# Optimization experiments

Hardware: AMD Instinct MI355X
Metric: run time of the kernel (lower is better)

## Reference

```python
import jax, jax.numpy as jnp
import numpy as np

# Dims: S strings, B batch, D bond dim, N=784 input sites, P=2 phys dim, L=10 labels
S, B, D, N, P, L = 4, 64, 32, 784, 2, 10
HALF = N // 2  # 392 sites on each side of the label node


def setup_inputs() -> dict:
    key = jax.random.key(0)
    ks = jax.random.split(key, 6)
    # scale chosen so each transfer-matrix step keeps vector norm ~O(1)
    std = (3.0 / (2.0 * D)) ** 0.5
    inputs = jax.random.uniform(ks[0], (B, N, P), dtype=jnp.float32)
    A_first = jax.random.normal(ks[1], (S, D, P), dtype=jnp.float32) * std          # node 0
    A_left = jax.random.normal(ks[2], (S, HALF - 1, D, P, D), dtype=jnp.float32) * std   # nodes 1..391
    A_label = jax.random.normal(ks[3], (S, D, L, D), dtype=jnp.float32) * std       # node 392 (open label edge)
    A_right = jax.random.normal(ks[4], (S, HALF - 1, D, P, D), dtype=jnp.float32) * std  # nodes 393..783
    A_last = jax.random.normal(ks[5], (S, D, P), dtype=jnp.float32) * std           # node 784
    return {"inputs": inputs, "A_first": A_first, "A_left": A_left,
            "A_label": A_label, "A_right": A_right, "A_last": A_last}


def reference(inputs, A_first, A_left, A_label, A_right, A_last):
    x = inputs  # (B, N, P); original reshapes each sample to (784, 2)
    # Contract physical legs with inputs -> per-site transfer matrices, site-major for scan
    Ml = jnp.einsum('snipj,bnp->nsbij', A_left, x[:, 1:HALF])      # (391, S, B, D, D)
    v0 = jnp.einsum('sdp,bp->sbd', A_first, x[:, 0])               # (S, B, D)

    def step_left(v, M):
        return jnp.einsum('sbi,sbij->sbj', v, M), None
    v, _ = jax.lax.scan(step_left, v0, Ml)                          # (S, B, D)

    T = jnp.einsum('sbd,sdlj->sblj', v, A_label)                    # (S, B, L, D)

    Mr = jnp.einsum('snipj,bnp->nsbij', A_right, x[:, HALF:N - 1])  # (391, S, B, D, D)
    r0 = jnp.einsum('sdp,bp->sbd', A_last, x[:, N - 1])             # (S, B, D)

    def step_right(r, M):
        return jnp.einsum('sbij,sbj->sbi', M, r), None
    r, _ = jax.lax.scan(step_right, r0, Mr, reverse=True)           # (S, B, D)

    out_per_string = jnp.einsum('sblj,sbj->sbl', T, r)              # (S, B, L)
    # forward multiplies the per-string 10-vectors elementwise (init ones)
    return jnp.prod(out_per_string, axis=0)                         # (B, L)
```

## Files before the change

### kernel.cpp

```cpp
#include <hip/hip_runtime.h>
#include <stdint.h>

#define S 4
#define B 64
#define D 32
#define N 784
#define P 2
#define L 10
#define HALF 392
#define NSTEP 391
#define NPAIR 196
#define SLICE 4096

typedef float f4 __attribute__((ext_vector_type(4)));

__device__ __forceinline__ float bcast(float v, int lane) {
    return __uint_as_float(__builtin_amdgcn_readlane(__float_as_uint(v), lane));
}

__global__ __launch_bounds__(256) void pair_kernel(
    const float* __restrict__ A_left, const float* __restrict__ A_right,
    const float* __restrict__ x,
    float* __restrict__ Wbuf, float* __restrict__ wtab)
{
    const int stream = blockIdx.x;
    const int t      = blockIdx.y;
    const int side   = stream >> 2, s = stream & 3;
    __shared__ float sA[2048], sB[2048];
    const int tid = threadIdx.x;
    const bool leftover = (t == 195);

    const float* As = (side ? A_right : A_left) + (size_t)s * (NSTEP * 2048);
    int ia, ib;
    if (side == 0) { ia = 2 * t; ib = 2 * t + 1; }
    else           { ia = 389 - 2 * t; ib = 390 - 2 * t; }
    if (leftover)  { ia = side ? 0 : 390; ib = ia; }

    const float4* ga = (const float4*)(As + (size_t)ia * 2048);
    const float4* gb = (const float4*)(As + (size_t)ib * 2048);
    ((float4*)sA)[tid] = ga[tid]; ((float4*)sA)[tid + 256] = ga[tid + 256];
    ((float4*)sB)[tid] = gb[tid]; ((float4*)sB)[tid + 256] = gb[tid + 256];
    __syncthreads();

    const int c = tid >> 6, rest = tid & 63, ff = rest >> 1, eh = rest & 1;
    const int a = c & 1, bb = c >> 1;
    float out[16];

    if (!leftover) {
        if (side == 0) {
            float col[32];
            #pragma unroll
            for (int k = 0; k < 32; ++k) col[k] = sB[k * 64 + bb * 32 + ff];
            #pragma unroll
            for (int e0 = 0; e0 < 16; ++e0) {
                const int e = eh * 16 + e0; float acc = 0.f;
                #pragma unroll
                for (int k = 0; k < 32; ++k)
                    acc = fmaf(sA[e * 64 + a * 32 + k], col[k], acc);
                out[e0] = acc;
            }
        } else {
            float row[32];
            #pragma unroll
            for (int k = 0; k < 32; ++k) row[k] = sA[ff * 64 + a * 32 + k];
            #pragma unroll
            for (int e0 = 0; e0 < 16; ++e0) {
                const int e = eh * 16 + e0; float acc = 0.f;
                #pragma unroll
                for (int k = 0; k < 32; ++k)
                    acc = fmaf(row[k], sB[k * 64 + bb * 32 + e], acc);
                out[e0] = acc;
            }
        }
    } else {
        #pragma unroll
        for (int e0 = 0; e0 < 16; ++e0) {
            const int e = eh * 16 + e0;
            out[e0] = (side == 0) ? sA[e * 64 + a * 32 + ff]
                                  : sA[ff * 64 + a * 32 + e];
        }
    }

    float* Wt = Wbuf + ((size_t)stream * NPAIR + t) * SLICE;
    #pragma unroll
    for (int q0 = 0; q0 < 4; ++q0) {
        const int qq = eh * 4 + q0;
        float4 val = make_float4(out[q0 * 4 + 0], out[q0 * 4 + 1],
                                 out[q0 * 4 + 2], out[q0 * 4 + 3]);
        ((float4*)Wt)[(bb * 8 + qq) * 64 + a * 32 + ff] = val;
    }

    if (stream < 2 && tid < 64) {
        const int sd = stream;
        const float2* x2 = (const float2*)x;
        float2 xa, xb;
        if (!leftover) {
            int na, nb;
            if (sd == 0) { na = 2 * t + 1; nb = 2 * t + 2; }
            else         { int ma = 389 - 2 * t; na = HALF + ma; nb = na + 1; }
            xa = x2[(size_t)tid * N + na];
            xb = x2[(size_t)tid * N + nb];
        } else {
            xa = x2[(size_t)tid * N + (sd ? HALF : 391)];
            xb = make_float2(1.f, 0.f);
        }
        float4 w = make_float4(xa.x * xb.x, xa.y * xb.x, xa.x * xb.y, xa.y * xb.y);
        ((float4*)wtab)[((size_t)sd * 64 + tid) * NPAIR + t] = w;
    }
}

#define GLOADX4(dst, voff, base, off) \
    asm volatile("global_load_dwordx4 %0, %1, %2 offset:" #off \
                 : "=v"(dst) : "v"(voff), "s"(base))

#define ISSUE_SLOT(SL) do { \
    GLOADX4(SL##0,  voff, base0, 0); GLOADX4(SL##1,  voff, base0, 1024); \
    GLOADX4(SL##2,  voff, base0, 2048); GLOADX4(SL##3,  voff, base0, 3072); \
    GLOADX4(SL##4,  voff, base1, 0); GLOADX4(SL##5,  voff, base1, 1024); \
    GLOADX4(SL##6,  voff, base1, 2048); GLOADX4(SL##7,  voff, base1, 3072); \
    GLOADX4(SL##8,  voff, base2, 0); GLOADX4(SL##9,  voff, base2, 1024); \
    GLOADX4(SL##10, voff, base2, 2048); GLOADX4(SL##11, voff, base2, 3072); \
    GLOADX4(SL##12, voff, base3, 0); GLOADX4(SL##13, voff, base3, 1024); \
    GLOADX4(SL##14, voff, base3, 2048); GLOADX4(SL##15, voff, base3, 3072); \
    voff += 16384; \
} while (0)

#define WAIT(n) do { \
    asm volatile("s_waitcnt vmcnt(" #n ")"); \
    __builtin_amdgcn_sched_barrier(0); \
} while (0)

#define FMAD2_1(RL_, RH_, aL0, aH0, aL1, aH1, E) do { \
    const float s_ = bcast(v0, E), t_ = bcast(v1, E); \
    aL0 = fmaf(RL_, s_, aL0); aH0 = fmaf(RH_, s_, aH0); \
    aL1 = fmaf(RL_, t_, aL1); aH1 = fmaf(RH_, t_, aH1); \
} while (0)

#define FMAD2(RqL, RqH, aL0, aH0, aL1, aH1, eb) \
    FMAD2_1(RqL.x, RqH.x, aL0, aH0, aL1, aH1, eb + 0); \
    FMAD2_1(RqL.y, RqH.y, aL0, aH0, aL1, aH1, eb + 1); \
    FMAD2_1(RqL.z, RqH.z, aL0, aH0, aL1, aH1, eb + 2); \
    FMAD2_1(RqL.w, RqH.w, aL0, aH0, aL1, aH1, eb + 3);

#define CONSUME_SLOT(SL, W0, W1) do { \
    float q00 = 0.f, q01 = 0.f, q02 = 0.f, q03 = 0.f; \
    float q10 = 0.f, q11 = 0.f, q12 = 0.f, q13 = 0.f; \
    FMAD2(SL##0, SL##8,  q00, q02, q10, q12, 0)  \
    FMAD2(SL##1, SL##9,  q00, q02, q10, q12, 4)  \
    FMAD2(SL##2, SL##10, q00, q02, q10, q12, 8)  \
    FMAD2(SL##3, SL##11, q00, q02, q10, q12, 12) \
    FMAD2(SL##4, SL##12, q01, q03, q11, q13, 16) \
    FMAD2(SL##5, SL##13, q01, q03, q11, q13, 20) \
    FMAD2(SL##6, SL##14, q01, q03, q11, q13, 24) \
    FMAD2(SL##7, SL##15, q01, q03, q11, q13, 28) \
    const float wl0 = c2 ? W0.y : W0.x, wh0 = c2 ? W0.w : W0.z; \
    const float wl1 = c2 ? W1.y : W1.x, wh1 = c2 ? W1.w : W1.z; \
    const float part0 = fmaf(wl0, q00 + q01, wh0 * (q02 + q03)); \
    const float part1 = fmaf(wl1, q10 + q11, wh1 * (q12 + q13)); \
    v0 = part0 + __shfl_xor(part0, 32); \
    v1 = part1 + __shfl_xor(part1, 32); \
} while (0)

__global__ __launch_bounds__(64, 1) void chain_kernel(
    const float* __restrict__ x,
    const float* __restrict__ A_first, const float* __restrict__ A_last,
    const float* __restrict__ Wbuf, const float* __restrict__ wtab,
    float* __restrict__ ws_v)
{
    __shared__ float4 lw[2 * NPAIR];

    const int lane = threadIdx.x, c2 = lane >> 5, f = lane & 31;
    const int blk = blockIdx.x, stream = blk & 7;
    const int side = stream >> 2, s = stream & 3;
    const int bp = blk >> 3;
    const int b0 = 2 * bp, b1 = 2 * bp + 1;

    const float4* wt4 = (const float4*)wtab;
    for (int i = lane; i < NPAIR; i += 64) {
        lw[2 * i]     = wt4[((size_t)side * 64 + b0) * NPAIR + i];
        lw[2 * i + 1] = wt4[((size_t)side * 64 + b1) * NPAIR + i];
    }

    const float2* x2 = (const float2*)x;
    const int site0 = side ? (N - 1) : 0;
    const float2 af  = ((const float2*)(side ? A_last : A_first))[s * D + f];
    const float2 xx0 = x2[(size_t)b0 * N + site0];
    const float2 xx1 = x2[(size_t)b1 * N + site0];
    float v0 = fmaf(af.x, xx0.x, af.y * xx0.y);
    float v1 = fmaf(af.x, xx1.x, af.y * xx1.y);

    const uint64_t wbase = (uint64_t)((const char*)Wbuf
                         + (size_t)stream * (NPAIR * SLICE) * 4);
    const uint64_t base0 = wbase, base1 = wbase + 4096;
    const uint64_t base2 = wbase + 8192, base3 = wbase + 12288;
    uint32_t voff = (uint32_t)lane * 16;

    f4 A0,A1,A2,A3,A4,A5,A6,A7,A8,A9,A10,A11,A12,A13,A14,A15;
    f4 B0,B1,B2,B3,B4,B5,B6,B7,B8,B9,B10,B11,B12,B13,B14,B15;

    ISSUE_SLOT(A);
    ISSUE_SLOT(B);
    float4 wA0 = lw[0], wA1 = lw[1];
    float4 wB0 = lw[2], wB1 = lw[3];

    for (int k = 0; k < 97; ++k) {
        WAIT(16); CONSUME_SLOT(A, wA0, wA1);
        ISSUE_SLOT(A);
        wA0 = lw[2 * (2 * k + 2)]; wA1 = lw[2 * (2 * k + 2) + 1];
        WAIT(16); CONSUME_SLOT(B, wB0, wB1);
        ISSUE_SLOT(B);
        wB0 = lw[2 * (2 * k + 3)]; wB1 = lw[2 * (2 * k + 3) + 1];
    }
    WAIT(16); CONSUME_SLOT(A, wA0, wA1);
    WAIT(0);  CONSUME_SLOT(B, wB0, wB1);

    if (lane < 32) {
        ws_v[(side * S + s) * (B * D) + b0 * D + f] = v0;
        ws_v[(side * S + s) * (B * D) + b1 * D + f] = v1;
    }
}

__global__ __launch_bounds__(64) void chain_fb(
    const float* __restrict__ x, const float* __restrict__ A_first,
    const float* __restrict__ A_left, const float* __restrict__ A_right,
    const float* __restrict__ A_last, float* __restrict__ ws_v)
{
    const int blk = blockIdx.x, pair = blk & 7, b = blk >> 3;
    const int side = pair >> 2, s = pair & 3;
    const int lane = threadIdx.x, p = lane >> 5, j = lane & 31;
    const float* xb = x + b * (N * P);
    float v;
    if (side == 0) {
        v = fmaf(A_first[s*D*P + j*P + 0], xb[0], A_first[s*D*P + j*P + 1] * xb[1]);
        const float* Abase = A_left + (size_t)s * (NSTEP * D * P * D);
        for (int n = 1; n <= NSTEP; ++n) {
            const float* M = Abase + (n - 1) * (D * P * D) + p * D + j;
            const float x0 = xb[n*P], x1 = xb[n*P + 1];
            float t0 = 0.f, t1 = 0.f;
            #pragma unroll
            for (int i = 0; i < D; i += 2) {
                t0 = fmaf(bcast(v, i),     M[i * (P*D)],       t0);
                t1 = fmaf(bcast(v, i + 1), M[(i + 1) * (P*D)], t1);
            }
            const float t = t0 + t1, o = __shfl_xor(t, 32);
            v = (p == 0) ? fmaf(x0, t, x1 * o) : fmaf(x1, t, x0 * o);
        }
    } else {
        v = fmaf(A_last[s*D*P + j*P + 0], xb[(N-1)*P], A_last[s*D*P + j*P + 1] * xb[(N-1)*P + 1]);
        const float* Abase = A_right + (size_t)s * (NSTEP * D * P * D);
        for (int m = NSTEP - 1; m >= 0; --m) {
            const float4* R4 = (const float4*)(Abase + m * (D*P*D) + j * (P*D) + p * D);
            const float x0 = xb[(HALF+m)*P], x1 = xb[(HALF+m)*P + 1];
            float t0 = 0.f, t1 = 0.f;
            #pragma unroll
            for (int q = 0; q < 8; ++q) {
                const float4 rv = R4[q];
                t0 = fmaf(rv.x, bcast(v, 4*q+0), t0);
                t1 = fmaf(rv.y, bcast(v, 4*q+1), t1);
                t0 = fmaf(rv.z, bcast(v, 4*q+2), t0);
                t1 = fmaf(rv.w, bcast(v, 4*q+3), t1);
            }
            const float t = t0 + t1, o = __shfl_xor(t, 32);
            v = (p == 0) ? fmaf(x0, t, x1 * o) : fmaf(x1, t, x0 * o);
        }
    }
    if (p == 0) ws_v[(side*S + s)*(B*D) + b*D + j] = v;
}

__global__ __launch_bounds__(64) void label_prod_kernel(
    const float* __restrict__ ws_v, const float* __restrict__ A_label,
    float* __restrict__ out)
{
    const int b = blockIdx.x;
    const int lane = threadIdx.x, h = lane >> 5, j = lane & 31;
    float pr0 = 1.f, pr1 = 1.f, pr2 = 1.f, pr3 = 1.f, pr4 = 1.f;

    #pragma unroll
    for (int s = 0; s < S; ++s) {
        const float vj = ws_v[(0 * S + s) * (B * D) + b * D + j];
        const float rj = ws_v[(1 * S + s) * (B * D) + b * D + j];
        #pragma unroll
        for (int q = 0; q < 5; ++q) {
            const int l = h * 5 + q;
            float w = 0.f;
            #pragma unroll
            for (int d = 0; d < D; ++d)
                w = fmaf(bcast(vj, d), A_label[((s * D + d) * L + l) * D + j], w);
            float c = w * rj;
            c += __shfl_xor(c, 1); c += __shfl_xor(c, 2); c += __shfl_xor(c, 4);
            c += __shfl_xor(c, 8); c += __shfl_xor(c, 16);
            if (q == 0) pr0 *= c; else if (q == 1) pr1 *= c;
            else if (q == 2) pr2 *= c; else if (q == 3) pr3 *= c; else pr4 *= c;
        }
    }
    if (j == 0) {
        out[b * L + h * 5 + 0] = pr0;
        out[b * L + h * 5 + 1] = pr1;
        out[b * L + h * 5 + 2] = pr2;
        out[b * L + h * 5 + 3] = pr3;
        out[b * L + h * 5 + 4] = pr4;
    }
}

extern "C" void kernel_launch(void* const* d_in, const int* in_sizes, int n_in,
                              void* d_out, int out_size, void* d_ws, size_t ws_size,
                              hipStream_t stream) {
    const float* x       = (const float*)d_in[0];
    const float* A_first = (const float*)d_in[1];
    const float* A_left  = (const float*)d_in[2];
    const float* A_label = (const float*)d_in[3];
    const float* A_right = (const float*)d_in[4];
    const float* A_last  = (const float*)d_in[5];
    float* out = (float*)d_out;

    float* ws_v = (float*)d_ws;
    float* wtab = ws_v + 2 * S * B * D;
    float* Wbuf = wtab + 2 * 64 * NPAIR * 4;
    const size_t need = (size_t)(16384 + 100352 + 8 * NPAIR * SLICE) * 4;

    if (ws_size >= need) {
        pair_kernel<<<dim3(8, NPAIR), dim3(256), 0, stream>>>(A_left, A_right, x, Wbuf, wtab);
        chain_kernel<<<dim3(256), dim3(64), 0, stream>>>(x, A_first, A_last, Wbuf, wtab, ws_v);
    } else {
        chain_fb<<<dim3(2 * S * B), dim3(64), 0, stream>>>(x, A_first, A_left, A_right, A_last, ws_v);
    }
    label_prod_kernel<<<dim3(B), dim3(64), 0, stream>>>(ws_v, A_label, out);
}
```

Measured before the change: 119.1 us.

## Stage transfer-matrix slices through LDS with async global_load_lds ring buffer

Replaces the register double-buffered global loads in the chain kernel with a 4-slot LDS ring buffer filled by global_load_lds direct-to-LDS copies, staged three slices ahead. Each step then reads its slice from LDS with ds_read_b128 and waits on lgkmcnt piecewise so the FMAs can overlap the LDS reads. The aim is deeper prefetch without the register pressure of holding two full slices in VGPRs, at the cost of 64KB of LDS per block and extra LDS read traffic. The weight pair values are now read directly with ds_read2_b32 instead of select logic.

```diff
diff --git a/kernel.cpp b/kernel.cpp
--- a/kernel.cpp
+++ b/kernel.cpp
@@ -13,6 +13,7 @@
 #define SLICE 4096
 
 typedef float f4 __attribute__((ext_vector_type(4)));
+typedef float f2 __attribute__((ext_vector_type(2)));
 
 __device__ __forceinline__ float bcast(float v, int lane) {
     return __uint_as_float(__builtin_amdgcn_readlane(__float_as_uint(v), lane));
@@ -109,25 +110,29 @@
     }
 }
 
-#define GLOADX4(dst, voff, base, off) \
-    asm volatile("global_load_dwordx4 %0, %1, %2 offset:" #off \
-                 : "=v"(dst) : "v"(voff), "s"(base))
-
-#define ISSUE_SLOT(SL) do { \
-    GLOADX4(SL##0,  voff, base0, 0); GLOADX4(SL##1,  voff, base0, 1024); \
-    GLOADX4(SL##2,  voff, base0, 2048); GLOADX4(SL##3,  voff, base0, 3072); \
-    GLOADX4(SL##4,  voff, base1, 0); GLOADX4(SL##5,  voff, base1, 1024); \
-    GLOADX4(SL##6,  voff, base1, 2048); GLOADX4(SL##7,  voff, base1, 3072); \
-    GLOADX4(SL##8,  voff, base2, 0); GLOADX4(SL##9,  voff, base2, 1024); \
-    GLOADX4(SL##10, voff, base2, 2048); GLOADX4(SL##11, voff, base2, 3072); \
-    GLOADX4(SL##12, voff, base3, 0); GLOADX4(SL##13, voff, base3, 1024); \
-    GLOADX4(SL##14, voff, base3, 2048); GLOADX4(SL##15, voff, base3, 3072); \
-    voff += 16384; \
-} while (0)
-
-#define WAIT(n) do { \
-    asm volatile("s_waitcnt vmcnt(" #n ")"); \
+#define WAITV(n) do { \
+    asm volatile("s_waitcnt vmcnt(" #n ")" ::: "memory"); \
     __builtin_amdgcn_sched_barrier(0); \
+} while (0)
+
+#define WAITL(n) do { \
+    asm volatile("s_waitcnt lgkmcnt(" #n ")" ::: "memory"); \
+    __builtin_amdgcn_sched_barrier(0); \
+} while (0)
+
+#define DSR(dst, OFF) \
+    asm volatile("ds_read_b128 %0, %1 offset:%c2" \
+                 : "=v"(dst) : "v"(sl_addr), "i"(OFF))
+
+#define STAGE(SLOTD) do { \
+    _Pragma("unroll") \
+    for (int c_ = 0; c_ < 16; ++c_) { \
+        __builtin_amdgcn_global_load_lds( \
+            (const __attribute__((address_space(1))) uint32_t*)(gsrc + goff + c_ * 1024), \
+            (__attribute__((address_space(3))) uint32_t*)(uintptr_t)((char*)lds_sl + (SLOTD) * 16384 + c_ * 1024), \
+            16, 0, 0); \
+    } \
+    goff += 16384; \
 } while (0)
 
 #define FMAD2_1(RL_, RH_, aL0, aH0, aL1, aH1, E) do { \
@@ -142,21 +147,33 @@
     FMAD2_1(RqL.z, RqH.z, aL0, aH0, aL1, aH1, eb + 2); \
     FMAD2_1(RqL.w, RqH.w, aL0, aH0, aL1, aH1, eb + 3);
 
-#define CONSUME_SLOT(SL, W0, W1) do { \
-    float q00 = 0.f, q01 = 0.f, q02 = 0.f, q03 = 0.f; \
-    float q10 = 0.f, q11 = 0.f, q12 = 0.f, q13 = 0.f; \
-    FMAD2(SL##0, SL##8,  q00, q02, q10, q12, 0)  \
-    FMAD2(SL##1, SL##9,  q00, q02, q10, q12, 4)  \
-    FMAD2(SL##2, SL##10, q00, q02, q10, q12, 8)  \
-    FMAD2(SL##3, SL##11, q00, q02, q10, q12, 12) \
-    FMAD2(SL##4, SL##12, q01, q03, q11, q13, 16) \
-    FMAD2(SL##5, SL##13, q01, q03, q11, q13, 20) \
-    FMAD2(SL##6, SL##14, q01, q03, q11, q13, 24) \
-    FMAD2(SL##7, SL##15, q01, q03, q11, q13, 28) \
-    const float wl0 = c2 ? W0.y : W0.x, wh0 = c2 ? W0.w : W0.z; \
-    const float wl1 = c2 ? W1.y : W1.x, wh1 = c2 ? W1.w : W1.z; \
-    const float part0 = fmaf(wl0, q00 + q01, wh0 * (q02 + q03)); \
-    const float part1 = fmaf(wl1, q10 + q11, wh1 * (q12 + q13)); \
+#define STEP(SLOT, WN, DO_STAGE) do { \
+    WAITV(WN); \
+    f4 d0,d1,d2,d3,d4,d5,d6,d7,d8,d9,d10,d11,d12,d13,d14,d15; \
+    f2 wa_, wb_; \
+    asm volatile("ds_read2_b32 %0, %1 offset0:0 offset1:2" : "=v"(wa_) : "v"(w_addr)); \
+    asm volatile("ds_read2_b32 %0, %1 offset0:4 offset1:6" : "=v"(wb_) : "v"(w_addr)); \
+    w_addr += 32; \
+    DSR(d0,  (SLOT)*16384 + 0);    DSR(d8,  (SLOT)*16384 + 8192);  \
+    DSR(d1,  (SLOT)*16384 + 1024); DSR(d9,  (SLOT)*16384 + 9216);  \
+    DSR(d2,  (SLOT)*16384 + 2048); DSR(d10, (SLOT)*16384 + 10240); \
+    DSR(d3,  (SLOT)*16384 + 3072); DSR(d11, (SLOT)*16384 + 11264); \
+    DSR(d4,  (SLOT)*16384 + 4096); DSR(d12, (SLOT)*16384 + 12288); \
+    DSR(d5,  (SLOT)*16384 + 5120); DSR(d13, (SLOT)*16384 + 13312); \
+    DSR(d6,  (SLOT)*16384 + 6144); DSR(d14, (SLOT)*16384 + 14336); \
+    DSR(d7,  (SLOT)*16384 + 7168); DSR(d15, (SLOT)*16384 + 15360); \
+    if (DO_STAGE) { STAGE((SLOT + 3) & 3); } \
+    float q00=0.f,q01=0.f,q02=0.f,q03=0.f,q10=0.f,q11=0.f,q12=0.f,q13=0.f; \
+    WAITL(14); FMAD2(d0, d8,  q00, q02, q10, q12, 0)  \
+    WAITL(12); FMAD2(d1, d9,  q00, q02, q10, q12, 4)  \
+    WAITL(10); FMAD2(d2, d10, q00, q02, q10, q12, 8)  \
+    WAITL(8);  FMAD2(d3, d11, q00, q02, q10, q12, 12) \
+    WAITL(6);  FMAD2(d4, d12, q01, q03, q11, q13, 16) \
+    WAITL(4);  FMAD2(d5, d13, q01, q03, q11, q13, 20) \
+    WAITL(2);  FMAD2(d6, d14, q01, q03, q11, q13, 24) \
+    WAITL(0);  FMAD2(d7, d15, q01, q03, q11, q13, 28) \
+    const float part0 = fmaf(wa_.x, q00 + q01, wa_.y * (q02 + q03)); \
+    const float part1 = fmaf(wb_.x, q10 + q11, wb_.y * (q12 + q13)); \
     v0 = part0 + __shfl_xor(part0, 32); \
     v1 = part1 + __shfl_xor(part1, 32); \
 } while (0)
@@ -167,6 +184,7 @@
     const float* __restrict__ Wbuf, const float* __restrict__ wtab,
     float* __restrict__ ws_v)
 {
+    __shared__ float  lds_sl[4 * SLICE];
     __shared__ float4 lw[2 * NPAIR];
 
     const int lane = threadIdx.x, c2 = lane >> 5, f = lane & 31;
@@ -189,30 +207,27 @@
     float v0 = fmaf(af.x, xx0.x, af.y * xx0.y);
     float v1 = fmaf(af.x, xx1.x, af.y * xx1.y);
 
-    const uint64_t wbase = (uint64_t)((const char*)Wbuf
-                         + (size_t)stream * (NPAIR * SLICE) * 4);
-    const uint64_t base0 = wbase, base1 = wbase + 4096;
-    const uint64_t base2 = wbase + 8192, base3 = wbase + 12288;
-    uint32_t voff = (uint32_t)lane * 16;
-
-    f4 A0,A1,A2,A3,A4,A5,A6,A7,A8,A9,A10,A11,A12,A13,A14,A15;
-    f4 B0,B1,B2,B3,B4,B5,B6,B7,B8,B9,B10,B11,B12,B13,B14,B15;
-
-    ISSUE_SLOT(A);
-    ISSUE_SLOT(B);
-    float4 wA0 = lw[0], wA1 = lw[1];
-    float4 wB0 = lw[2], wB1 = lw[3];
-
-    for (int k = 0; k < 97; ++k) {
-        WAIT(16); CONSUME_SLOT(A, wA0, wA1);
-        ISSUE_SLOT(A);
-        wA0 = lw[2 * (2 * k + 2)]; wA1 = lw[2 * (2 * k + 2) + 1];
-        WAIT(16); CONSUME_SLOT(B, wB0, wB1);
-        ISSUE_SLOT(B);
-        wB0 = lw[2 * (2 * k + 3)]; wB1 = lw[2 * (2 * k + 3) + 1];
-    }
-    WAIT(16); CONSUME_SLOT(A, wA0, wA1);
-    WAIT(0);  CONSUME_SLOT(B, wB0, wB1);
+    asm volatile("s_waitcnt vmcnt(0) lgkmcnt(0)" ::: "memory");
+    __builtin_amdgcn_sched_barrier(0);
+
+    const char* gsrc = (const char*)Wbuf
+                     + (size_t)stream * (NPAIR * SLICE) * 4 + (size_t)lane * 16;
+    uint32_t goff = 0;
+    uint32_t sl_addr = (uint32_t)(uintptr_t)&lds_sl[0] + (uint32_t)lane * 16;
+    uint32_t w_addr  = (uint32_t)(uintptr_t)&lw[0] + (uint32_t)c2 * 4;
+
+    STAGE(0); STAGE(1); STAGE(2);
+
+    for (int k = 0; k < 48; ++k) {
+        STEP(0, 32, 1);
+        STEP(1, 32, 1);
+        STEP(2, 32, 1);
+        STEP(3, 32, 1);
+    }
+    STEP(0, 32, 1);
+    STEP(1, 32, 0);
+    STEP(2, 16, 0);
+    STEP(3, 0,  0);
 
     if (lane < 32) {
         ws_v[(side * S + s) * (B * D) + b0 * D + f] = v0;
```

Measured after the change: 150.8 us. +26.6%, slower.

## Split chain kernel across two waves with LDS exchange and triple-buffered loads

Applied to the files above, without the earlier changes.

The chain kernel now runs two wavefronts per block. Each wave loads and contracts half of every pair matrix slice, and the partial results are exchanged through double-buffered LDS with a barrier each step. The prefetch pipeline moves from two slots of 16 loads to three slots of 8. It also uses packed f2 FMAs and reverses the pair kernel's block order so the slices consumed first are produced last, perhaps helping the L2 cache. The aim is to halve the per-wave serial FMA and load latency on the dependent chain, at the cost of a block barrier and LDS round trip per step.

```diff
diff --git a/kernel.cpp b/kernel.cpp
--- a/kernel.cpp
+++ b/kernel.cpp
@@ -13,6 +13,7 @@
 #define SLICE 4096
 
 typedef float f4 __attribute__((ext_vector_type(4)));
+typedef float f2 __attribute__((ext_vector_type(2)));
 
 __device__ __forceinline__ float bcast(float v, int lane) {
     return __uint_as_float(__builtin_amdgcn_readlane(__float_as_uint(v), lane));
@@ -24,7 +25,7 @@
     float* __restrict__ Wbuf, float* __restrict__ wtab)
 {
     const int stream = blockIdx.x;
-    const int t      = blockIdx.y;
+    const int t      = (NPAIR - 1) - blockIdx.y;
     const int side   = stream >> 2, s = stream & 3;
     __shared__ float sA[2048], sB[2048];
     const int tid = threadIdx.x;
@@ -113,73 +114,88 @@
     asm volatile("global_load_dwordx4 %0, %1, %2 offset:" #off \
                  : "=v"(dst) : "v"(voff), "s"(base))
 
-#define ISSUE_SLOT(SL) do { \
-    GLOADX4(SL##0,  voff, base0, 0); GLOADX4(SL##1,  voff, base0, 1024); \
-    GLOADX4(SL##2,  voff, base0, 2048); GLOADX4(SL##3,  voff, base0, 3072); \
-    GLOADX4(SL##4,  voff, base1, 0); GLOADX4(SL##5,  voff, base1, 1024); \
-    GLOADX4(SL##6,  voff, base1, 2048); GLOADX4(SL##7,  voff, base1, 3072); \
-    GLOADX4(SL##8,  voff, base2, 0); GLOADX4(SL##9,  voff, base2, 1024); \
-    GLOADX4(SL##10, voff, base2, 2048); GLOADX4(SL##11, voff, base2, 3072); \
-    GLOADX4(SL##12, voff, base3, 0); GLOADX4(SL##13, voff, base3, 1024); \
-    GLOADX4(SL##14, voff, base3, 2048); GLOADX4(SL##15, voff, base3, 3072); \
+#define ISSUE8(SL) do { \
+    GLOADX4(SL##0, voff, base0, 0);    GLOADX4(SL##1, voff, base0, 1024); \
+    GLOADX4(SL##2, voff, base0, 2048); GLOADX4(SL##3, voff, base0, 3072); \
+    GLOADX4(SL##4, voff, base1, 0);    GLOADX4(SL##5, voff, base1, 1024); \
+    GLOADX4(SL##6, voff, base1, 2048); GLOADX4(SL##7, voff, base1, 3072); \
     voff += 16384; \
 } while (0)
 
-#define WAIT(n) do { \
-    asm volatile("s_waitcnt vmcnt(" #n ")"); \
+#define WAITV(n) do { \
+    asm volatile("s_waitcnt vmcnt(" #n ")" ::: "memory"); \
     __builtin_amdgcn_sched_barrier(0); \
 } while (0)
 
-#define FMAD2_1(RL_, RH_, aL0, aH0, aL1, aH1, E) do { \
-    const float s_ = bcast(v0, E), t_ = bcast(v1, E); \
-    aL0 = fmaf(RL_, s_, aL0); aH0 = fmaf(RH_, s_, aH0); \
-    aL1 = fmaf(RL_, t_, aL1); aH1 = fmaf(RH_, t_, aH1); \
-} while (0)
-
-#define FMAD2(RqL, RqH, aL0, aH0, aL1, aH1, eb) \
-    FMAD2_1(RqL.x, RqH.x, aL0, aH0, aL1, aH1, eb + 0); \
-    FMAD2_1(RqL.y, RqH.y, aL0, aH0, aL1, aH1, eb + 1); \
-    FMAD2_1(RqL.z, RqH.z, aL0, aH0, aL1, aH1, eb + 2); \
-    FMAD2_1(RqL.w, RqH.w, aL0, aH0, aL1, aH1, eb + 3);
-
-#define CONSUME_SLOT(SL, W0, W1) do { \
-    float q00 = 0.f, q01 = 0.f, q02 = 0.f, q03 = 0.f; \
-    float q10 = 0.f, q11 = 0.f, q12 = 0.f, q13 = 0.f; \
-    FMAD2(SL##0, SL##8,  q00, q02, q10, q12, 0)  \
-    FMAD2(SL##1, SL##9,  q00, q02, q10, q12, 4)  \
-    FMAD2(SL##2, SL##10, q00, q02, q10, q12, 8)  \
-    FMAD2(SL##3, SL##11, q00, q02, q10, q12, 12) \
-    FMAD2(SL##4, SL##12, q01, q03, q11, q13, 16) \
-    FMAD2(SL##5, SL##13, q01, q03, q11, q13, 20) \
-    FMAD2(SL##6, SL##14, q01, q03, q11, q13, 24) \
-    FMAD2(SL##7, SL##15, q01, q03, q11, q13, 28) \
-    const float wl0 = c2 ? W0.y : W0.x, wh0 = c2 ? W0.w : W0.z; \
-    const float wl1 = c2 ? W1.y : W1.x, wh1 = c2 ? W1.w : W1.z; \
-    const float part0 = fmaf(wl0, q00 + q01, wh0 * (q02 + q03)); \
-    const float part1 = fmaf(wl1, q10 + q11, wh1 * (q12 + q13)); \
-    v0 = part0 + __shfl_xor(part0, 32); \
-    v1 = part1 + __shfl_xor(part1, 32); \
-} while (0)
-
-__global__ __launch_bounds__(64, 1) void chain_kernel(
+#define WAITL(n) do { \
+    asm volatile("s_waitcnt lgkmcnt(" #n ")" ::: "memory"); \
+    __builtin_amdgcn_sched_barrier(0); \
+} while (0)
+
+#define CHUNK(Rq, EB) do { \
+    const f2 l0 = __builtin_shufflevector(Rq, Rq, 0, 1); \
+    const f2 l1 = __builtin_shufflevector(Rq, Rq, 2, 3); \
+    f2 sa0, sa1, sb0, sb1; \
+    sa0.x = bcast(v0, EB + 0); sa0.y = bcast(v0, EB + 1); \
+    sa1.x = bcast(v0, EB + 2); sa1.y = bcast(v0, EB + 3); \
+    sb0.x = bcast(v1, EB + 0); sb0.y = bcast(v1, EB + 1); \
+    sb1.x = bcast(v1, EB + 2); sb1.y = bcast(v1, EB + 3); \
+    QA0 = __builtin_elementwise_fma(l0, sa0, QA0); \
+    QB0 = __builtin_elementwise_fma(l1, sa1, QB0); \
+    QA1 = __builtin_elementwise_fma(l0, sb0, QA1); \
+    QB1 = __builtin_elementwise_fma(l1, sb1, QB1); \
+} while (0)
+
+#define STEP(SL, WN, DO_ISSUE) do { \
+    WAITV(WN); \
+    f2 QA0 = {0.f,0.f}, QB0 = {0.f,0.f}, QA1 = {0.f,0.f}, QB1 = {0.f,0.f}; \
+    CHUNK(SL##0, 0);  CHUNK(SL##1, 4);  CHUNK(SL##2, 8);  CHUNK(SL##3, 12); \
+    CHUNK(SL##4, 16); CHUNK(SL##5, 20); CHUNK(SL##6, 24); CHUNK(SL##7, 28); \
+    if (DO_ISSUE) { ISSUE8(SL); } \
+    WAITL(0);   \
+    const float sum0 = (QA0.x + QA0.y) + (QB0.x + QB0.y); \
+    const float sum1 = (QA1.x + QA1.y) + (QB1.x + QB1.y); \
+    float part0 = wreg.x * sum0; \
+    float part1 = wreg.y * sum1; \
+    part0 += __shfl_xor(part0, 32); \
+    part1 += __shfl_xor(part1, 32); \
+    f2 pp; pp.x = part0; pp.y = part1; \
+    asm volatile("ds_write_b64 %0, %1" :: "v"(ewr), "v"(pp) : "memory"); \
+    WAITL(0); \
+    __builtin_amdgcn_s_barrier(); \
+    f2 oth; \
+    asm volatile("ds_read_b64 %0, %1" : "=v"(oth) : "v"(er)); \
+    asm volatile("ds_read2_b32 %0, %1 offset0:0 offset1:4" : "=v"(wreg) : "v"(w_addr)); \
+    w_addr += 32; ewr += ptog; er += ptog; ptog = -ptog; \
+    WAITL(1);   \
+    v0 = part0 + oth.x; \
+    v1 = part1 + oth.y; \
+} while (0)
+
+__global__ __launch_bounds__(128, 1) void chain_kernel(
     const float* __restrict__ x,
     const float* __restrict__ A_first, const float* __restrict__ A_last,
     const float* __restrict__ Wbuf, const float* __restrict__ wtab,
     float* __restrict__ ws_v)
 {
-    __shared__ float4 lw[2 * NPAIR];
-
-    const int lane = threadIdx.x, c2 = lane >> 5, f = lane & 31;
-    const int blk = blockIdx.x, stream = blk & 7;
+    __shared__ float4 lw[2 * (NPAIR + 2)];
+    __shared__ f2 exch[2][2][32];
+
+    const int tid  = threadIdx.x;
+    const int w    = tid >> 6;
+    const int lane = tid & 63;
+    const int c2   = lane >> 5, f = lane & 31;
+    const int blk  = blockIdx.x, stream = blk & 7;
     const int side = stream >> 2, s = stream & 3;
-    const int bp = blk >> 3;
-    const int b0 = 2 * bp, b1 = 2 * bp + 1;
+    const int bp   = blk >> 3;
+    const int b0   = 2 * bp, b1 = 2 * bp + 1;
 
     const float4* wt4 = (const float4*)wtab;
-    for (int i = lane; i < NPAIR; i += 64) {
+    for (int i = tid; i < NPAIR; i += 128) {
         lw[2 * i]     = wt4[((size_t)side * 64 + b0) * NPAIR + i];
         lw[2 * i + 1] = wt4[((size_t)side * 64 + b1) * NPAIR + i];
     }
+    __syncthreads();
 
     const float2* x2 = (const float2*)x;
     const int site0 = side ? (N - 1) : 0;
@@ -189,32 +205,42 @@
     float v0 = fmaf(af.x, xx0.x, af.y * xx0.y);
     float v1 = fmaf(af.x, xx1.x, af.y * xx1.y);
 
-    const uint64_t wbase = (uint64_t)((const char*)Wbuf
-                         + (size_t)stream * (NPAIR * SLICE) * 4);
-    const uint64_t base0 = wbase, base1 = wbase + 4096;
-    const uint64_t base2 = wbase + 8192, base3 = wbase + 12288;
+    asm volatile("s_waitcnt vmcnt(0) lgkmcnt(0)" ::: "memory");
+    __builtin_amdgcn_sched_barrier(0);
+
+    const uint64_t wb = (uint64_t)((const char*)Wbuf
+                      + (size_t)stream * (NPAIR * SLICE) * 4 + (size_t)w * 8192);
+    const uint32_t wb_lo = __builtin_amdgcn_readfirstlane((uint32_t)wb);
+    const uint32_t wb_hi = __builtin_amdgcn_readfirstlane((uint32_t)(wb >> 32));
+    const uint64_t base0 = ((uint64_t)wb_hi << 32) | wb_lo;
+    const uint64_t base1 = base0 + 4096;
     uint32_t voff = (uint32_t)lane * 16;
 
-    f4 A0,A1,A2,A3,A4,A5,A6,A7,A8,A9,A10,A11,A12,A13,A14,A15;
-    f4 B0,B1,B2,B3,B4,B5,B6,B7,B8,B9,B10,B11,B12,B13,B14,B15;
-
-    ISSUE_SLOT(A);
-    ISSUE_SLOT(B);
-    float4 wA0 = lw[0], wA1 = lw[1];
-    float4 wB0 = lw[2], wB1 = lw[3];
-
-    for (int k = 0; k < 97; ++k) {
-        WAIT(16); CONSUME_SLOT(A, wA0, wA1);
-        ISSUE_SLOT(A);
-        wA0 = lw[2 * (2 * k + 2)]; wA1 = lw[2 * (2 * k + 2) + 1];
-        WAIT(16); CONSUME_SLOT(B, wB0, wB1);
-        ISSUE_SLOT(B);
-        wB0 = lw[2 * (2 * k + 3)]; wB1 = lw[2 * (2 * k + 3) + 1];
-    }
-    WAIT(16); CONSUME_SLOT(A, wA0, wA1);
-    WAIT(0);  CONSUME_SLOT(B, wB0, wB1);
-
-    if (lane < 32) {
+    uint32_t w_addr = (uint32_t)(uintptr_t)&lw[0] + (uint32_t)(c2 + 2 * w) * 4;
+    uint32_t ewr = (uint32_t)(uintptr_t)&exch[0][w][f];
+    uint32_t er  = (uint32_t)(uintptr_t)&exch[0][1 - w][f];
+    int ptog = 512;
+
+    f4 KA0,KA1,KA2,KA3,KA4,KA5,KA6,KA7;
+    f4 KB0,KB1,KB2,KB3,KB4,KB5,KB6,KB7;
+    f4 KC0,KC1,KC2,KC3,KC4,KC5,KC6,KC7;
+
+    ISSUE8(KA); ISSUE8(KB); ISSUE8(KC);
+    f2 wreg;
+    asm volatile("ds_read2_b32 %0, %1 offset0:0 offset1:4" : "=v"(wreg) : "v"(w_addr));
+    w_addr += 32;
+
+    for (int k = 0; k < 64; ++k) {
+        STEP(KA, 16, 1);
+        STEP(KB, 16, 1);
+        STEP(KC, 16, 1);
+    }
+    STEP(KA, 16, 1);
+    STEP(KB, 16, 0);
+    STEP(KC, 8,  0);
+    STEP(KA, 0,  0);
+
+    if (tid < 32) {
         ws_v[(side * S + s) * (B * D) + b0 * D + f] = v0;
         ws_v[(side * S + s) * (B * D) + b1 * D + f] = v1;
     }
@@ -320,7 +346,7 @@
 
     if (ws_size >= need) {
         pair_kernel<<<dim3(8, NPAIR), dim3(256), 0, stream>>>(A_left, A_right, x, Wbuf, wtab);
-        chain_kernel<<<dim3(256), dim3(64), 0, stream>>>(x, A_first, A_last, Wbuf, wtab, ws_v);
+        chain_kernel<<<dim3(256), dim3(128), 0, stream>>>(x, A_first, A_last, Wbuf, wtab, ws_v);
     } else {
         chain_fb<<<dim3(2 * S * B), dim3(64), 0, stream>>>(x, A_first, A_left, A_right, A_last, ws_v);
     }
```

Result: slower. 121.5 us (+2.0%).
